# Performance work log

Hardware: AMD Instinct MI355X
Metric: run time of the kernel (lower is better)

Reference implementation:

```python
import jax, jax.numpy as jnp
import numpy as np

B, T, D = 8, 1024, 512
H = 8
F_OUT = D // H          # 64 per head
ALPHA = 0.2             # LeakyReLU slope in GAT
MASK_RATE = 0.3
GAMMA = 0.0625          # DistanceAdj gamma
BIAS = 0.2              # DistanceAdj bias
LN_EPS = 1e-5
NEG_INF = -9e15
L2_EPS = 1e-12          # F.normalize eps


def setup_inputs() -> dict:
    key = jax.random.key(0)
    ks = jax.random.split(key, 8)
    return {
        "x": jax.random.normal(ks[0], (B, T, D), jnp.float32),
        "W": jax.random.normal(ks[1], (H, D, F_OUT), jnp.float32) * 0.05,
        "a_src": jax.random.normal(ks[2], (H, F_OUT), jnp.float32) * 0.05,
        "a_dst": jax.random.normal(ks[3], (H, F_OUT), jnp.float32) * 0.05,
        "W2": jax.random.normal(ks[4], (D, D), jnp.float32) * 0.02,
        "b2": jnp.zeros((D,), jnp.float32),
        "ln_g": jnp.ones((D,), jnp.float32),
        "ln_b": jnp.zeros((D,), jnp.float32),
    }


def _distance_adj(batch, t):
    # DistanceAdj: Gaussian kernel over temporal index distance, shared across batch
    idx = jnp.arange(t, dtype=jnp.float32)
    d2 = (idx[:, None] - idx[None, :]) ** 2
    adj = jnp.exp(-GAMMA * d2 - BIAS)                      # [T, T]
    return jnp.broadcast_to(adj[None], (batch, t, t))      # [B, T, T]


def reference(x, W, a_src, a_dst, W2, b2, ln_g, ln_b):
    b, t, d = x.shape
    adj = _distance_adj(b, t)

    # top-k magnitude node selection -> row/col union mask (index_fill loop)
    k = int(MASK_RATE * t)
    mags = jnp.linalg.norm(x, axis=2)                      # [B, T]
    _, topk = jax.lax.top_k(mags, k)                       # [B, k]
    sel = jnp.zeros((b, t), bool).at[jnp.arange(b)[:, None], topk].set(True)
    mask = sel[:, :, None] | sel[:, None, :]               # rows OR cols filled
    adj = jnp.where(mask, adj, 0.0)

    # GAT multi-head attention (dense masked form, dropout=0 at eval)
    Wh = jnp.einsum("btd,hdf->bhtf", x, W)                 # [B,H,T,F']
    e_src = jnp.einsum("bhtf,hf->bht", Wh, a_src)
    e_dst = jnp.einsum("bhtf,hf->bht", Wh, a_dst)
    e = jax.nn.leaky_relu(e_src[..., :, None] + e_dst[..., None, :], ALPHA)
    e = jnp.where(adj[:, None] > 0, e, NEG_INF)            # masked logits
    attn = jax.nn.softmax(e, axis=-1)                      # [B,H,T,T]
    hp = jnp.einsum("bhts,bhsf->bhtf", attn, Wh)
    hp = jax.nn.elu(hp)                                    # concat=True -> elu per head
    tmp = hp.transpose(0, 2, 1, 3).reshape(b, t, d)        # concat heads -> [B,T,512]

    # signed-sqrt + F.normalize (default dim=1 -> over T axis)
    tmp = jnp.sqrt(jax.nn.relu(tmp)) - jnp.sqrt(jax.nn.relu(-tmp))
    nrm = jnp.linalg.norm(tmp, axis=1, keepdims=True)      # [B,1,D]
    tmp = tmp / jnp.maximum(nrm, L2_EPS)

    # residual linear + LayerNorm + permute
    y = x + tmp @ W2 + b2
    mu = jnp.mean(y, axis=-1, keepdims=True)
    var = jnp.mean((y - mu) ** 2, axis=-1, keepdims=True)
    y = (y - mu) / jnp.sqrt(var + LN_EPS) * ln_g + ln_b
    return y.transpose(0, 2, 1)                            # [B, D, T]
```

## Files before the change

kernel.cpp:

```cpp
#include <hip/hip_runtime.h>
#include <hip/hip_bf16.h>

typedef unsigned short u16;
typedef short bf16x8 __attribute__((ext_vector_type(8)));
typedef float f32x4 __attribute__((ext_vector_type(4)));
typedef int   i32x4 __attribute__((ext_vector_type(4)));

#define NB 8
#define NT 1024
#define ND 512
#define KSEL 307
#define PSTR 152
#define TSTR 136

__device__ __forceinline__ float bf2f(u16 u){
  union { unsigned int i; float f; } c; c.i = ((unsigned int)u) << 16; return c.f;
}
__device__ __forceinline__ u16 f2bf(float f){
  __hip_bfloat16 h = __float2bfloat16(f);
  u16 u; __builtin_memcpy(&u, &h, 2); return u;
}

__global__ void k_select(const float* __restrict__ mags, int* __restrict__ sel,
                         float* __restrict__ cn){
  __shared__ float sm[NT];
  int b = blockIdx.x;
  int tid = threadIdx.x;
  if (tid < 32) cn[b * ND + blockIdx.y * 32 + tid] = 0.f;
  for (int i = tid; i < NT; i += 256) sm[i] = mags[b * NT + i];
  __syncthreads();
  int tl = tid >> 2, tq = tid & 3;
  int t = blockIdx.y * 64 + tl;
  float m = sm[t];
  int cnt = 0;
  int s0 = tq * 256;
  for (int s = s0; s < s0 + 256; s++){
    float v = sm[s];
    cnt += (v > m) || (v == m && s < t);
  }
  cnt += __shfl_xor(cnt, 1, 64);
  cnt += __shfl_xor(cnt, 2, 64);
  if (tq == 0) sel[b * NT + t] = (cnt < KSEL) ? 1 : 0;
}

__launch_bounds__(256, 3)
__global__ void k_gemm_wh(const float* __restrict__ x, const float* __restrict__ Wf,
                          const float* __restrict__ a_src, const float* __restrict__ a_dst,
                          u16* __restrict__ WhT, float* __restrict__ es, float* __restrict__ ed,
                          float* __restrict__ mags){
  __shared__ u16 smem[8704];
  u16* As = smem;
  u16* Bs = smem + 5120;
  int m0 = blockIdx.x * 128;
  int h  = blockIdx.y;
  int tid = threadIdx.x;
  int wv = tid >> 6, lane = tid & 63;
  int quad = lane >> 4, lr = lane & 15;
  f32x4 acc[2][4] = {};
  float sq[2] = {0.f, 0.f};
  for (int kt = 0; kt < 512; kt += 32){
    __syncthreads();
#pragma unroll
    for (int i = 0; i < 2; i++){
      int e = tid * 8 + i * 2048;
      int r = e >> 5, c = e & 31;
      const float* xa = &x[(m0 + r) * 512 + kt + c];
      f32x4 u0 = *(const f32x4*)xa;
      f32x4 u1 = *(const f32x4*)(xa + 4);
      u16 pk[8];
#pragma unroll
      for (int q = 0; q < 4; q++){
        sq[i] += u0[q]*u0[q] + u1[q]*u1[q];
        pk[q] = f2bf(u0[q]); pk[4+q] = f2bf(u1[q]);
      }
      *(bf16x8*)&As[r*40 + c] = *(const bf16x8*)pk;
    }
    {
      int e = tid * 8;
      int r = e >> 5, c = e & 31;
      const float* wsrc = &Wf[((size_t)h << 15) + (size_t)(kt + c) * 64 + r];
      u16 pk[8];
#pragma unroll
      for (int q = 0; q < 8; q++) pk[q] = f2bf(wsrc[q * 64]);
      *(bf16x8*)&Bs[r*40 + c] = *(const bf16x8*)pk;
    }
    __syncthreads();
    bf16x8 af[2], bfr[4];
#pragma unroll
    for (int i = 0; i < 2; i++) af[i] = *(const bf16x8*)&As[(wv*32 + i*16 + lr)*40 + quad*8];
#pragma unroll
    for (int i = 0; i < 4; i++) bfr[i] = *(const bf16x8*)&Bs[(i*16 + lr)*40 + quad*8];
#pragma unroll
    for (int mi = 0; mi < 2; mi++)
#pragma unroll
      for (int ni = 0; ni < 4; ni++)
        acc[mi][ni] = __builtin_amdgcn_mfma_f32_16x16x32_bf16(af[mi], bfr[ni], acc[mi][ni], 0, 0, 0);
  }
  if (blockIdx.y == 0){
#pragma unroll
    for (int i = 0; i < 2; i++){
      float s = sq[i];
      s += __shfl_xor(s, 1, 64);
      s += __shfl_xor(s, 2, 64);
      if ((tid & 3) == 0) mags[m0 + i*64 + (tid >> 2)] = sqrtf(s);
    }
  }
  float asv[4], adv[4];
#pragma unroll
  for (int ni = 0; ni < 4; ni++){
    asv[ni] = a_src[h*64 + ni*16 + lr];
    adv[ni] = a_dst[h*64 + ni*16 + lr];
  }
#pragma unroll
  for (int mi = 0; mi < 2; mi++)
#pragma unroll
    for (int r = 0; r < 4; r++){
      float pes = 0.f, ped = 0.f;
#pragma unroll
      for (int ni = 0; ni < 4; ni++){
        pes += acc[mi][ni][r] * asv[ni];
        ped += acc[mi][ni][r] * adv[ni];
      }
#pragma unroll
      for (int mofs = 1; mofs < 16; mofs <<= 1){
        pes += __shfl_xor(pes, mofs, 64);
        ped += __shfl_xor(ped, mofs, 64);
      }
      if (lr == 0){
        int rowg = m0 + wv*32 + mi*16 + quad*4 + r;
        int bb_ = rowg >> 10, tt = rowg & 1023;
        es[(bb_ * 8 + h) * NT + tt] = pes;
        ed[(bb_ * 8 + h) * NT + tt] = ped;
      }
    }
  __syncthreads();
  u16* Tr = smem;
#pragma unroll
  for (int mi = 0; mi < 2; mi++)
#pragma unroll
    for (int ni = 0; ni < 4; ni++){
      int fl = ni*16 + lr;
      int tl = wv*32 + mi*16 + quad*4;
#pragma unroll
      for (int r = 0; r < 4; r++) Tr[fl*TSTR + tl + r] = f2bf(acc[mi][ni][r]);
    }
  __syncthreads();
  int f = tid >> 2, seg = tid & 3;
  int b_ = m0 >> 10;
  u16* dst = &WhT[(b_ * 512 + h * 64 + f) * NT + (m0 & 1023) + seg*32];
  const u16* srcp = &Tr[f*TSTR + seg*32];
#pragma unroll
  for (int k8 = 0; k8 < 4; k8++)
    *(bf16x8*)(dst + k8*8) = *(const bf16x8*)(srcp + k8*8);
}

__launch_bounds__(256)
__global__ void k_attn(const u16* __restrict__ WhT, const float* __restrict__ es,
                       const float* __restrict__ ed, const int* __restrict__ sel,
                       u16* __restrict__ t2b, float* __restrict__ cn){
  __shared__ u16 P[64 * PSTR];
  __shared__ float edw[144];
  __shared__ int   selw[144];
  __shared__ float esw[64];
  __shared__ float swv[64];
  int bh = blockIdx.x;
  int b = bh >> 3;
  int t0 = blockIdx.y * 64;
  int tid = threadIdx.x;
  int wv = tid >> 6, lane = tid & 63;
  int quad = lane >> 4, lr = lane & 15;
  int s_base = t0 - 40;
  for (int i = tid; i < 144; i += 256){
    int s = s_base + i;
    bool ok = (s >= 0 && s < NT);
    edw[i]  = ok ? ed[bh * NT + s] : 0.f;
    selw[i] = ok ? sel[b * NT + s] : 0;
  }
  if (tid < 64) esw[tid] = es[bh * NT + t0 + tid];
  {
    i32x4 z = {};
    for (int i = lane; i < 304; i += 64){
      int r16 = i / 19, c16 = i - r16 * 19;
      *(i32x4*)&P[(16*wv + r16) * PSTR + c16 * 8] = z;
    }
  }
  __syncthreads();
  {
    int tl = 16*wv + (lane >> 2);
    int q = lane & 3;
    float e_t = esw[tl];
    int sel_t = selw[tl + 40];
    float part = 0.f;
    for (int j = q; j <= 80; j += 4){
      int sw = tl + j;
      int s = s_base + sw;
      float w = 0.f;
      if (s >= 0 && s < NT && (sel_t | selw[sw])){
        float v = e_t + edw[sw];
        v = v > 0.f ? v : 0.2f * v;
        v = fminf(v, 60.f);
        w = bf2f(f2bf(__expf(v)));
      }
      part += w;
      if (w != 0.f) P[tl * PSTR + sw] = f2bf(w);
    }
    part += __shfl_xor(part, 1, 64);
    part += __shfl_xor(part, 2, 64);
    if (q == 0) swv[tl] = part;
  }
  f32x4 acc[4] = {};
  const u16* vbase = WhT + (bh * 64) * NT;
#pragma unroll
  for (int ks = 0; ks < 96; ks += 32){
    bf16x8 afr = *(const bf16x8*)&P[(16*wv + lr) * PSTR + 16*wv + ks + quad*8];
    int tb = s_base + 16*wv + ks + quad*8;
    bool ok = (tb >= 0) && (tb < NT);
    bf16x8 zf = {};
#pragma unroll
    for (int jn = 0; jn < 4; jn++){
      bf16x8 bfr = ok ? *(const bf16x8*)&vbase[(16*jn + lr) * NT + tb] : zf;
      acc[jn] = __builtin_amdgcn_mfma_f32_16x16x32_bf16(afr, bfr, acc[jn], 0, 0, 0);
    }
  }
#pragma unroll
  for (int jn = 0; jn < 4; jn++){
    float ssum = 0.f;
#pragma unroll
    for (int r = 0; r < 4; r++){
      int t_loc = 16*wv + quad*4 + r;
      float sw_ = swv[t_loc];
      float hp = acc[jn][r] / (sw_ > 0.f ? sw_ : 1.f);
      hp = hp > 0.f ? hp : (__expf(hp) - 1.f);
      float o = hp >= 0.f ? sqrtf(hp) : -sqrtf(-hp);
      ssum += o * o;
      t2b[(b * NT + t0 + t_loc) * ND + (bh & 7) * 64 + 16*jn + lr] = f2bf(o);
    }
    ssum += __shfl_xor(ssum, 16, 64);
    ssum += __shfl_xor(ssum, 32, 64);
    if (quad == 0) atomicAdd(&cn[b * ND + (bh & 7) * 64 + 16*jn + lr], ssum);
  }
}

__launch_bounds__(256, 3)
__global__ void k_gemm2(const u16* __restrict__ A, const float* __restrict__ W2f,
                        const float* __restrict__ xres, const float* __restrict__ b2,
                        const float* __restrict__ cn, float* __restrict__ Y,
                        float* __restrict__ rsum, float* __restrict__ rqsum){
  __shared__ u16 As[128 * 40];
  __shared__ u16 Bs[64 * 40];
  __shared__ float scl[512];
  int m0 = blockIdx.x * 128, n0 = blockIdx.y * 64;
  int tid = threadIdx.x;
  int wv = tid >> 6, lane = tid & 63;
  int quad = lane >> 4, lr = lane & 15;
  int bb0 = (m0 >> 10) << 9;
  for (int i = tid; i < 512; i += 256){
    float nv = sqrtf(cn[bb0 + i]);
    scl[i] = 1.f / fmaxf(nv, 1e-12f);
  }
  f32x4 acc[2][4] = {};
  for (int kt = 0; kt < 512; kt += 32){
    __syncthreads();
#pragma unroll
    for (int i = 0; i < 2; i++){
      int e = tid * 8 + i * 2048;
      int r = e >> 5, c = e & 31;
      bf16x8 raw = *(const bf16x8*)&A[(m0 + r) * 512 + kt + c];
      u16 pk[8];
#pragma unroll
      for (int q = 0; q < 8; q++)
        pk[q] = f2bf(bf2f((u16)raw[q]) * scl[kt + c + q]);
      *(bf16x8*)&As[r*40 + c] = *(const bf16x8*)pk;
    }
    {
      int e = tid * 8;
      int r = e >> 5, c = e & 31;
      const float* wsrc = &W2f[(size_t)(kt + c) * 512 + n0 + r];
      u16 pk[8];
#pragma unroll
      for (int q = 0; q < 8; q++) pk[q] = f2bf(wsrc[q * 512]);
      *(bf16x8*)&Bs[r*40 + c] = *(const bf16x8*)pk;
    }
    __syncthreads();
    bf16x8 af[2], bfr[4];
#pragma unroll
    for (int i = 0; i < 2; i++) af[i] = *(const bf16x8*)&As[(wv*32 + i*16 + lr)*40 + quad*8];
#pragma unroll
    for (int i = 0; i < 4; i++) bfr[i] = *(const bf16x8*)&Bs[(i*16 + lr)*40 + quad*8];
#pragma unroll
    for (int mi = 0; mi < 2; mi++)
#pragma unroll
      for (int ni = 0; ni < 4; ni++)
        acc[mi][ni] = __builtin_amdgcn_mfma_f32_16x16x32_bf16(af[mi], bfr[ni], acc[mi][ni], 0, 0, 0);
  }
  float b2v[4];
#pragma unroll
  for (int ni = 0; ni < 4; ni++) b2v[ni] = b2[n0 + ni*16 + lr];
#pragma unroll
  for (int mi = 0; mi < 2; mi++){
    int rgb = m0 + wv*32 + mi*16 + quad*4;
#pragma unroll
    for (int r = 0; r < 4; r++){
      int row = rgb + r;
      float rs = 0.f, rq = 0.f;
#pragma unroll
      for (int ni = 0; ni < 4; ni++){
        int cg = n0 + ni*16 + lr;
        int idx = row * 512 + cg;
        float yv = acc[mi][ni][r] + xres[idx] + b2v[ni];
        Y[idx] = yv;
        rs += yv; rq += yv * yv;
      }
#pragma unroll
      for (int m2 = 1; m2 < 16; m2 <<= 1){
        rs += __shfl_xor(rs, m2, 64);
        rq += __shfl_xor(rq, m2, 64);
      }
      if (lr == 0){
        atomicAdd(&rsum[row], rs);
        atomicAdd(&rqsum[row], rq);
      }
    }
  }
}

__global__ void k_outln(const float* __restrict__ Y, const float* __restrict__ rsum,
                        const float* __restrict__ rqsum, const float* __restrict__ g,
                        const float* __restrict__ bb, float* __restrict__ out){
  __shared__ float mus[64], rss[64];
  __shared__ float tile[64 * 65];
  int t0 = blockIdx.x * 64, b = blockIdx.y;
  int cbase = blockIdx.z * 128;
  int tid = threadIdx.x;
  if (tid < 64){
    int row = b * NT + t0 + tid;
    float m = rsum[row] * (1.f/512.f);
    float var = rqsum[row] * (1.f/512.f) - m * m;
    mus[tid] = m;
    rss[tid] = 1.f / sqrtf(var + 1e-5f);
  }
  __syncthreads();
  int j = tid & 63, i0 = tid >> 6;
  for (int c0 = cbase; c0 < cbase + 128; c0 += 64){
#pragma unroll
    for (int k = 0; k < 16; k++){
      int i = i0 + k * 4;
      float v = (Y[(b * NT + t0 + i) * ND + c0 + j] - mus[i]) * rss[i] * g[c0 + j] + bb[c0 + j];
      tile[i * 65 + j] = v;
    }
    __syncthreads();
#pragma unroll
    for (int k = 0; k < 16; k++){
      int jj = i0 + k * 4;
      out[(b * ND + c0 + jj) * NT + t0 + j] = tile[j * 65 + jj];
    }
    __syncthreads();
  }
}

extern "C" void kernel_launch(void* const* d_in, const int* in_sizes, int n_in,
                              void* d_out, int out_size, void* d_ws, size_t ws_size,
                              hipStream_t stream) {
  (void)in_sizes; (void)n_in; (void)out_size; (void)ws_size;
  const float* x     = (const float*)d_in[0];
  const float* W     = (const float*)d_in[1];
  const float* a_src = (const float*)d_in[2];
  const float* a_dst = (const float*)d_in[3];
  const float* W2    = (const float*)d_in[4];
  const float* b2    = (const float*)d_in[5];
  const float* ln_g  = (const float*)d_in[6];
  const float* ln_b  = (const float*)d_in[7];
  char* ws = (char*)d_ws;
  int*   sel   = (int*)  (ws + 256);
  float* mags  = (float*)(ws + 33024);
  float* es    = (float*)(ws + 1124608);
  float* ed    = (float*)(ws + 1386752);
  float* cn    = (float*)(ws + 1648896);
  float* rsum  = (float*)(ws + 1665280);
  float* rqsum = (float*)(ws + 1698048);
  u16*   WhT   = (u16*)  (ws + 2097152);
  u16*   t2b   = (u16*)  (ws + 18874368);
  float* Y     = (float*)(ws + 2097152);
  float* out   = (float*)d_out;

  hipMemsetAsync(rsum, 0, 65536, stream);
  k_gemm_wh  <<<dim3(64, 8), 256, 0, stream>>>(x, W, a_src, a_dst, WhT, es, ed, mags);
  k_select   <<<dim3(NB, 16), 256, 0, stream>>>(mags, sel, cn);
  k_attn     <<<dim3(64, 16), 256, 0, stream>>>(WhT, es, ed, sel, t2b, cn);
  k_gemm2    <<<dim3(64, 8), 256, 0, stream>>>(t2b, W2, x, b2, cn, Y, rsum, rqsum);
  k_outln    <<<dim3(16, NB, 4), 256, 0, stream>>>(Y, rsum, rqsum, ln_g, ln_b, out);
}
```

Baseline: 158.2 us.

## Double GEMM K-tile to 64 and store pre-LayerNorm Y in bf16

Result: slower. 174.8 us (+10.5%).

```diff
diff --git a/kernel.cpp b/kernel.cpp
--- a/kernel.cpp
+++ b/kernel.cpp
@@ -12,6 +12,7 @@
 #define KSEL 307
 #define PSTR 152
 #define TSTR 136
+#define GSTR 72
 
 __device__ __forceinline__ float bf2f(u16 u){
   union { unsigned int i; float f; } c; c.i = ((unsigned int)u) << 16; return c.f;
@@ -48,22 +49,22 @@
                           const float* __restrict__ a_src, const float* __restrict__ a_dst,
                           u16* __restrict__ WhT, float* __restrict__ es, float* __restrict__ ed,
                           float* __restrict__ mags){
-  __shared__ u16 smem[8704];
+  __shared__ u16 smem[192 * GSTR];
   u16* As = smem;
-  u16* Bs = smem + 5120;
+  u16* Bs = smem + 128 * GSTR;
   int m0 = blockIdx.x * 128;
   int h  = blockIdx.y;
   int tid = threadIdx.x;
   int wv = tid >> 6, lane = tid & 63;
   int quad = lane >> 4, lr = lane & 15;
   f32x4 acc[2][4] = {};
-  float sq[2] = {0.f, 0.f};
-  for (int kt = 0; kt < 512; kt += 32){
-    __syncthreads();
-#pragma unroll
-    for (int i = 0; i < 2; i++){
+  float sq[4] = {0.f, 0.f, 0.f, 0.f};
+  for (int kt = 0; kt < 512; kt += 64){
+    __syncthreads();
+#pragma unroll
+    for (int i = 0; i < 4; i++){
       int e = tid * 8 + i * 2048;
-      int r = e >> 5, c = e & 31;
+      int r = e >> 6, c = e & 63;
       const float* xa = &x[(m0 + r) * 512 + kt + c];
       f32x4 u0 = *(const f32x4*)xa;
       f32x4 u1 = *(const f32x4*)(xa + 4);
@@ -73,36 +74,41 @@
         sq[i] += u0[q]*u0[q] + u1[q]*u1[q];
         pk[q] = f2bf(u0[q]); pk[4+q] = f2bf(u1[q]);
       }
-      *(bf16x8*)&As[r*40 + c] = *(const bf16x8*)pk;
-    }
-    {
-      int e = tid * 8;
-      int r = e >> 5, c = e & 31;
+      *(bf16x8*)&As[r*GSTR + c] = *(const bf16x8*)pk;
+    }
+#pragma unroll
+    for (int i = 0; i < 2; i++){
+      int e = tid * 8 + i * 2048;
+      int r = e >> 6, c = e & 63;
       const float* wsrc = &Wf[((size_t)h << 15) + (size_t)(kt + c) * 64 + r];
       u16 pk[8];
 #pragma unroll
       for (int q = 0; q < 8; q++) pk[q] = f2bf(wsrc[q * 64]);
-      *(bf16x8*)&Bs[r*40 + c] = *(const bf16x8*)pk;
-    }
-    __syncthreads();
-    bf16x8 af[2], bfr[4];
-#pragma unroll
-    for (int i = 0; i < 2; i++) af[i] = *(const bf16x8*)&As[(wv*32 + i*16 + lr)*40 + quad*8];
-#pragma unroll
-    for (int i = 0; i < 4; i++) bfr[i] = *(const bf16x8*)&Bs[(i*16 + lr)*40 + quad*8];
-#pragma unroll
-    for (int mi = 0; mi < 2; mi++)
-#pragma unroll
-      for (int ni = 0; ni < 4; ni++)
-        acc[mi][ni] = __builtin_amdgcn_mfma_f32_16x16x32_bf16(af[mi], bfr[ni], acc[mi][ni], 0, 0, 0);
+      *(bf16x8*)&Bs[r*GSTR + c] = *(const bf16x8*)pk;
+    }
+    __syncthreads();
+#pragma unroll
+    for (int ko = 0; ko < 64; ko += 32){
+      bf16x8 af[2], bfr[4];
+#pragma unroll
+      for (int i = 0; i < 2; i++) af[i] = *(const bf16x8*)&As[(wv*32 + i*16 + lr)*GSTR + ko + quad*8];
+#pragma unroll
+      for (int i = 0; i < 4; i++) bfr[i] = *(const bf16x8*)&Bs[(i*16 + lr)*GSTR + ko + quad*8];
+#pragma unroll
+      for (int mi = 0; mi < 2; mi++)
+#pragma unroll
+        for (int ni = 0; ni < 4; ni++)
+          acc[mi][ni] = __builtin_amdgcn_mfma_f32_16x16x32_bf16(af[mi], bfr[ni], acc[mi][ni], 0, 0, 0);
+    }
   }
   if (blockIdx.y == 0){
 #pragma unroll
-    for (int i = 0; i < 2; i++){
+    for (int i = 0; i < 4; i++){
       float s = sq[i];
       s += __shfl_xor(s, 1, 64);
       s += __shfl_xor(s, 2, 64);
-      if ((tid & 3) == 0) mags[m0 + i*64 + (tid >> 2)] = sqrtf(s);
+      s += __shfl_xor(s, 4, 64);
+      if ((tid & 7) == 0) mags[m0 + i*32 + (tid >> 3)] = sqrtf(s);
     }
   }
   float asv[4], adv[4];
@@ -244,11 +250,12 @@
 __launch_bounds__(256, 3)
 __global__ void k_gemm2(const u16* __restrict__ A, const float* __restrict__ W2f,
                         const float* __restrict__ xres, const float* __restrict__ b2,
-                        const float* __restrict__ cn, float* __restrict__ Y,
+                        const float* __restrict__ cn, u16* __restrict__ Yb,
                         float* __restrict__ rsum, float* __restrict__ rqsum){
-  __shared__ u16 As[128 * 40];
-  __shared__ u16 Bs[64 * 40];
+  __shared__ u16 smem[192 * GSTR];
   __shared__ float scl[512];
+  u16* As = smem;
+  u16* Bs = smem + 128 * GSTR;
   int m0 = blockIdx.x * 128, n0 = blockIdx.y * 64;
   int tid = threadIdx.x;
   int wv = tid >> 6, lane = tid & 63;
@@ -259,39 +266,43 @@
     scl[i] = 1.f / fmaxf(nv, 1e-12f);
   }
   f32x4 acc[2][4] = {};
-  for (int kt = 0; kt < 512; kt += 32){
-    __syncthreads();
+  for (int kt = 0; kt < 512; kt += 64){
+    __syncthreads();
+#pragma unroll
+    for (int i = 0; i < 4; i++){
+      int e = tid * 8 + i * 2048;
+      int r = e >> 6, c = e & 63;
+      bf16x8 raw = *(const bf16x8*)&A[(m0 + r) * 512 + kt + c];
+      u16 pk[8];
+#pragma unroll
+      for (int q = 0; q < 8; q++)
+        pk[q] = f2bf(bf2f((u16)raw[q]) * scl[kt + c + q]);
+      *(bf16x8*)&As[r*GSTR + c] = *(const bf16x8*)pk;
+    }
 #pragma unroll
     for (int i = 0; i < 2; i++){
       int e = tid * 8 + i * 2048;
-      int r = e >> 5, c = e & 31;
-      bf16x8 raw = *(const bf16x8*)&A[(m0 + r) * 512 + kt + c];
-      u16 pk[8];
-#pragma unroll
-      for (int q = 0; q < 8; q++)
-        pk[q] = f2bf(bf2f((u16)raw[q]) * scl[kt + c + q]);
-      *(bf16x8*)&As[r*40 + c] = *(const bf16x8*)pk;
-    }
-    {
-      int e = tid * 8;
-      int r = e >> 5, c = e & 31;
+      int r = e >> 6, c = e & 63;
       const float* wsrc = &W2f[(size_t)(kt + c) * 512 + n0 + r];
       u16 pk[8];
 #pragma unroll
       for (int q = 0; q < 8; q++) pk[q] = f2bf(wsrc[q * 512]);
-      *(bf16x8*)&Bs[r*40 + c] = *(const bf16x8*)pk;
-    }
-    __syncthreads();
-    bf16x8 af[2], bfr[4];
-#pragma unroll
-    for (int i = 0; i < 2; i++) af[i] = *(const bf16x8*)&As[(wv*32 + i*16 + lr)*40 + quad*8];
-#pragma unroll
-    for (int i = 0; i < 4; i++) bfr[i] = *(const bf16x8*)&Bs[(i*16 + lr)*40 + quad*8];
-#pragma unroll
-    for (int mi = 0; mi < 2; mi++)
-#pragma unroll
-      for (int ni = 0; ni < 4; ni++)
-        acc[mi][ni] = __builtin_amdgcn_mfma_f32_16x16x32_bf16(af[mi], bfr[ni], acc[mi][ni], 0, 0, 0);
+      *(bf16x8*)&Bs[r*GSTR + c] = *(const bf16x8*)pk;
+    }
+    __syncthreads();
+#pragma unroll
+    for (int ko = 0; ko < 64; ko += 32){
+      bf16x8 af[2], bfr[4];
+#pragma unroll
+      for (int i = 0; i < 2; i++) af[i] = *(const bf16x8*)&As[(wv*32 + i*16 + lr)*GSTR + ko + quad*8];
+#pragma unroll
+      for (int i = 0; i < 4; i++) bfr[i] = *(const bf16x8*)&Bs[(i*16 + lr)*GSTR + ko + quad*8];
+#pragma unroll
+      for (int mi = 0; mi < 2; mi++)
+#pragma unroll
+        for (int ni = 0; ni < 4; ni++)
+          acc[mi][ni] = __builtin_amdgcn_mfma_f32_16x16x32_bf16(af[mi], bfr[ni], acc[mi][ni], 0, 0, 0);
+    }
   }
   float b2v[4];
 #pragma unroll
@@ -308,7 +319,7 @@
         int cg = n0 + ni*16 + lr;
         int idx = row * 512 + cg;
         float yv = acc[mi][ni][r] + xres[idx] + b2v[ni];
-        Y[idx] = yv;
+        Yb[idx] = f2bf(yv);
         rs += yv; rq += yv * yv;
       }
 #pragma unroll
@@ -324,7 +335,7 @@
   }
 }
 
-__global__ void k_outln(const float* __restrict__ Y, const float* __restrict__ rsum,
+__global__ void k_outln(const u16* __restrict__ Yb, const float* __restrict__ rsum,
                         const float* __restrict__ rqsum, const float* __restrict__ g,
                         const float* __restrict__ bb, float* __restrict__ out){
   __shared__ float mus[64], rss[64];
@@ -345,7 +356,7 @@
 #pragma unroll
     for (int k = 0; k < 16; k++){
       int i = i0 + k * 4;
-      float v = (Y[(b * NT + t0 + i) * ND + c0 + j] - mus[i]) * rss[i] * g[c0 + j] + bb[c0 + j];
+      float v = (bf2f(Yb[(b * NT + t0 + i) * ND + c0 + j]) - mus[i]) * rss[i] * g[c0 + j] + bb[c0 + j];
       tile[i * 65 + j] = v;
     }
     __syncthreads();
@@ -380,13 +391,13 @@
   float* rqsum = (float*)(ws + 1698048);
   u16*   WhT   = (u16*)  (ws + 2097152);
   u16*   t2b   = (u16*)  (ws + 18874368);
-  float* Y     = (float*)(ws + 2097152);
+  u16*   Yb    = (u16*)  (ws + 2097152);
   float* out   = (float*)d_out;
 
   hipMemsetAsync(rsum, 0, 65536, stream);
   k_gemm_wh  <<<dim3(64, 8), 256, 0, stream>>>(x, W, a_src, a_dst, WhT, es, ed, mags);
   k_select   <<<dim3(NB, 16), 256, 0, stream>>>(mags, sel, cn);
   k_attn     <<<dim3(64, 16), 256, 0, stream>>>(WhT, es, ed, sel, t2b, cn);
-  k_gemm2    <<<dim3(64, 8), 256, 0, stream>>>(t2b, W2, x, b2, cn, Y, rsum, rqsum);
-  k_outln    <<<dim3(16, NB, 4), 256, 0, stream>>>(Y, rsum, rqsum, ln_g, ln_b, out);
-}
+  k_gemm2    <<<dim3(64, 8), 256, 0, stream>>>(t2b, W2, x, b2, cn, Yb, rsum, rqsum);
+  k_outln    <<<dim3(16, NB, 4), 256, 0, stream>>>(Yb, rsum, rqsum, ln_g, ln_b, out);
+}
```
